# Performance work log

Measured on AMD Instinct MI355X. Metric: run time of the kernel, lower is better.

## Reference

```python
import jax, jax.numpy as jnp
import numpy as np

EPS = 1e-12  # matches torch F.normalize default eps


def _l2norm(x):
    n = jnp.linalg.norm(x, axis=-1, keepdims=True)
    return x / jnp.maximum(n, EPS)


def setup_inputs() -> dict:
    key = jax.random.key(0)
    k1, k2, k3, k4 = jax.random.split(key, 4)
    B, N, Lq, Ld, D = 64, 16, 32, 256, 128
    query_rep = jax.random.normal(k1, (B, Lq, D), jnp.float32)
    doc_reps = jax.random.normal(k2, (B, N, Ld, D), jnp.float32)
    doc_mask = jax.random.randint(k3, (B, N, Ld), 0, 2).astype(jnp.int32)
    labels = jax.random.normal(k4, (B, 2 * N), jnp.float32)
    return {"query_rep": query_rep, "doc_reps": doc_reps,
            "doc_mask": doc_mask, "labels": labels}


def reference(query_rep, doc_reps, doc_mask, labels):
    # ColBERT MaxSim: normalize query tokens (no mask, as in original),
    # mask+normalize doc tokens, bmm, max over doc tokens, sum over query tokens.
    q = _l2norm(query_rep)                                   # [B,Lq,D]
    d = _l2norm(doc_reps * doc_mask[..., None].astype(doc_reps.dtype))  # [B,N,Ld,D]
    tok = jnp.einsum('bqd,bnld->bnql', q, d)                 # [B,N,Lq,Ld]
    scores = tok.max(axis=-1).sum(axis=-1)                   # [B,N]

    # Pairwise ranking loss
    N = scores.shape[1]
    ys = labels[:, :N]
    idx = labels[:, N:]
    diffs = jnp.triu(scores[:, :, None] - scores[:, None, :])    # [B,N,N], lower tri zeroed
    weights = jnp.abs(idx[:, :, None] - idx[:, None, :])
    pairs = (ys[:, :, None] - ys[:, None, :]) > 0
    losses = jnp.log1p(jnp.exp(-diffs)) * weights
    return jnp.sum(jnp.where(pairs, losses, 0.0))
```

## Files before the change

### kernel.cpp

```cpp
#include <hip/hip_runtime.h>
#include <cmath>

#define EPSN 1e-12f

typedef _Float16 half8 __attribute__((ext_vector_type(8)));
typedef float f32x4 __attribute__((ext_vector_type(4)));

__global__ __launch_bounds__(256, 4) void scores_kernel(
    const float* __restrict__ qr, const float* __restrict__ doc,
    const int* __restrict__ mask, float* __restrict__ pmax) {
    __shared__ __align__(16) char Aimg[16384];
    __shared__ __align__(16) char Bimg[16384];
    __shared__ float ssPart[256];
    __shared__ float invS[128];
    __shared__ int   compactS[128];
    __shared__ int   cntW[2];
    __shared__ float wq[4][32];

    int t = threadIdx.x, g = blockIdx.x;
    int bn = g >> 1, h = g & 1, b = g >> 5;
    int w = t >> 6, lane = t & 63, col = lane & 15;

    int row = t >> 3, jb = t & 7;
    const float4* qsrc = (const float4*)(qr + ((size_t)b * 32 + row) * 128 + jb * 16);
    float4 v0 = qsrc[0], v1 = qsrc[1], v2 = qsrc[2], v3 = qsrc[3];

    int myMask = 0;
    if (t < 128) myMask = mask[bn * 256 + h * 128 + t];
    unsigned long long bal = __ballot(myMask != 0);
    if (t < 128 && lane == 0) cntW[w] = __popcll(bal);
    __syncthreads();
    int cnt = cntW[0] + cntW[1];
    if (myMask) {
        int prefix = __popcll(bal & ((1ull << lane) - 1));
        int basec = (w == 1) ? cntW[0] : 0;
        compactS[basec + prefix] = t;
    }
    __syncthreads();

    int s = t & 127, kh = t >> 7;
    bool real = (s < cnt);
    int tokc = real ? compactS[s] : 0;

    const float4* dsrc = (const float4*)(doc + ((size_t)bn * 256 + h * 128 + tokc) * 128) + kh * 4;
    float4 rA0, rA1, rA2, rA3, rB0, rB1, rB2, rB3, rC0, rC1, rC2, rC3;
    if (real) {
        rA0 = dsrc[0];  rA1 = dsrc[1];  rA2 = dsrc[2],  rA3 = dsrc[3];
        rB0 = dsrc[8];  rB1 = dsrc[9];  rB2 = dsrc[10]; rB3 = dsrc[11];
    }

    {
        float ss = v0.x*v0.x + v0.y*v0.y + v0.z*v0.z + v0.w*v0.w
                 + v1.x*v1.x + v1.y*v1.y + v1.z*v1.z + v1.w*v1.w
                 + v2.x*v2.x + v2.y*v2.y + v2.z*v2.z + v2.w*v2.w
                 + v3.x*v3.x + v3.y*v3.y + v3.z*v3.z + v3.w*v3.w;
        ss += __shfl_xor(ss, 1); ss += __shfl_xor(ss, 2); ss += __shfl_xor(ss, 4);
        float inv = 1.0f / fmaxf(sqrtf(ss), EPSN);
        int qt = row >> 4, kstep = jb >> 1;
        float4 vv[4] = { v0, v1, v2, v3 };
#pragma unroll
        for (int khh = 0; khh < 2; ++khh) {
            float xs[8] = { vv[2*khh].x,   vv[2*khh].y,   vv[2*khh].z,   vv[2*khh].w,
                            vv[2*khh+1].x, vv[2*khh+1].y, vv[2*khh+1].z, vv[2*khh+1].w };
            half8 hh, hl;
#pragma unroll
            for (int e = 0; e < 8; ++e) {
                float x = xs[e] * inv;
                _Float16 hv = (_Float16)x;
                hh[e] = hv;
                hl[e] = (_Float16)(x - (float)hv);
            }
            int quad = (jb & 1) * 2 + khh;
            int base = ((qt * 4 + kstep) * 2) * 1024 + ((row & 15) + quad * 16) * 16;
            *(half8*)(Aimg + base)        = hh;
            *(half8*)(Aimg + base + 1024) = hl;
        }
    }
    asm volatile("s_waitcnt lgkmcnt(0)" ::: "memory");
    __builtin_amdgcn_s_barrier();

    f32x4 acc[2][2];
    f32x4 zero = {0.f, 0.f, 0.f, 0.f};
    acc[0][0] = zero; acc[0][1] = zero; acc[1][0] = zero; acc[1][1] = zero;
    float ss_d = 0.f;

    int tile8 = s >> 4;
    int bo_base = tile8 * 2048 + (2 * kh) * 256 + (s & 15) * 16;

#define CHUNK(C, P0, P1, P2, P3, N0, N1, N2, N3, PREF, ISLAST) do {           \
    if ((PREF) && real) {                                                     \
        N0 = dsrc[(C + 2) * 8 + 0]; N1 = dsrc[(C + 2) * 8 + 1];               \
        N2 = dsrc[(C + 2) * 8 + 2]; N3 = dsrc[(C + 2) * 8 + 3];               \
    }                                                                         \
    if (real) {                                                               \
        ss_d += P0.x*P0.x + P0.y*P0.y + P0.z*P0.z + P0.w*P0.w;                \
        ss_d += P1.x*P1.x + P1.y*P1.y + P1.z*P1.z + P1.w*P1.w;                \
        ss_d += P2.x*P2.x + P2.y*P2.y + P2.z*P2.z + P2.w*P2.w;                \
        ss_d += P3.x*P3.x + P3.y*P3.y + P3.z*P3.z + P3.w*P3.w;                \
        float xa[8] = { P0.x, P0.y, P0.z, P0.w, P1.x, P1.y, P1.z, P1.w };     \
        float xb[8] = { P2.x, P2.y, P2.z, P2.w, P3.x, P3.y, P3.z, P3.w };     \
        half8 hha, hla, hhb, hlb;                                             \
        _Pragma("unroll")                                                     \
        for (int e = 0; e < 8; ++e) {                                         \
            float x = xa[e]; _Float16 hv = (_Float16)x;                       \
            hha[e] = hv; hla[e] = (_Float16)(x - (float)hv);                  \
            float y = xb[e]; _Float16 hw = (_Float16)y;                       \
            hhb[e] = hw; hlb[e] = (_Float16)(y - (float)hw);                  \
        }                                                                     \
        *(half8*)(Bimg + bo_base)              = hha;                         \
        *(half8*)(Bimg + bo_base + 1024)       = hla;                         \
        *(half8*)(Bimg + bo_base + 256)        = hhb;                         \
        *(half8*)(Bimg + bo_base + 256 + 1024) = hlb;                         \
    } else if ((C) == 0) {                                                    \
        half8 hz = {0,0,0,0,0,0,0,0};                                         \
        *(half8*)(Bimg + bo_base)              = hz;                          \
        *(half8*)(Bimg + bo_base + 1024)       = hz;                          \
        *(half8*)(Bimg + bo_base + 256)        = hz;                          \
        *(half8*)(Bimg + bo_base + 256 + 1024) = hz;                          \
    }                                                                         \
    if (ISLAST) ssPart[t] = ss_d;                                             \
    asm volatile("s_waitcnt lgkmcnt(0)" ::: "memory");                        \
    __builtin_amdgcn_s_barrier();                                             \
    if ((ISLAST) && t < 128) {                                                \
        float sst = ssPart[t] + ssPart[t + 128];                              \
        invS[t] = (t < cnt) ? (1.0f / fmaxf(sqrtf(sst), EPSN)) : 0.0f;        \
    }                                                                         \
    {                                                                         \
        int lo = lane << 4;                                                   \
        half8 a0h = *(const half8*)(Aimg + (((C) * 2 + 0) << 10) + lo);       \
        half8 a0l = *(const half8*)(Aimg + (((C) * 2 + 1) << 10) + lo);       \
        half8 a1h = *(const half8*)(Aimg + (((4 + (C)) * 2 + 0) << 10) + lo); \
        half8 a1l = *(const half8*)(Aimg + (((4 + (C)) * 2 + 1) << 10) + lo); \
        _Pragma("unroll")                                                     \
        for (int nt = 0; nt < 2; ++nt) {                                      \
            int tile = w * 2 + nt;                                            \
            half8 bh = *(const half8*)(Bimg + tile * 2048 + lo);              \
            half8 bl = *(const half8*)(Bimg + tile * 2048 + 1024 + lo);       \
            acc[0][nt] = __builtin_amdgcn_mfma_f32_16x16x32_f16(a0l, bh, acc[0][nt], 0, 0, 0); \
            acc[0][nt] = __builtin_amdgcn_mfma_f32_16x16x32_f16(a0h, bl, acc[0][nt], 0, 0, 0); \
            acc[0][nt] = __builtin_amdgcn_mfma_f32_16x16x32_f16(a0h, bh, acc[0][nt], 0, 0, 0); \
            acc[1][nt] = __builtin_amdgcn_mfma_f32_16x16x32_f16(a1l, bh, acc[1][nt], 0, 0, 0); \
            acc[1][nt] = __builtin_amdgcn_mfma_f32_16x16x32_f16(a1h, bl, acc[1][nt], 0, 0, 0); \
            acc[1][nt] = __builtin_amdgcn_mfma_f32_16x16x32_f16(a1h, bh, acc[1][nt], 0, 0, 0); \
        }                                                                     \
    }                                                                         \
    asm volatile("s_waitcnt lgkmcnt(0)" ::: "memory");                        \
    __builtin_amdgcn_s_barrier();                                             \
} while (0)

    CHUNK(0, rA0, rA1, rA2, rA3, rC0, rC1, rC2, rC3, 1, false);
    CHUNK(1, rB0, rB1, rB2, rB3, rA0, rA1, rA2, rA3, 1, false);
    CHUNK(2, rC0, rC1, rC2, rC3, rB0, rB1, rB2, rB3, 0, false);
    CHUNK(3, rA0, rA1, rA2, rA3, rB0, rB1, rB2, rB3, 0, true);
#undef CHUNK

    float inv0 = invS[w * 32 + col];
    float inv1 = invS[w * 32 + 16 + col];
    float m8[8];
#pragma unroll
    for (int qt = 0; qt < 2; ++qt)
#pragma unroll
        for (int rr = 0; rr < 4; ++rr)
            m8[qt * 4 + rr] = fmaxf(acc[qt][0][rr] * inv0, acc[qt][1][rr] * inv1);
#pragma unroll
    for (int off = 1; off < 16; off <<= 1)
#pragma unroll
        for (int i = 0; i < 8; ++i) m8[i] = fmaxf(m8[i], __shfl_xor(m8[i], off));
    if (col == 0) {
        int rg = lane >> 4;
#pragma unroll
        for (int qt = 0; qt < 2; ++qt)
#pragma unroll
            for (int rr = 0; rr < 4; ++rr) wq[w][qt * 16 + rg * 4 + rr] = m8[qt * 4 + rr];
    }
    __syncthreads();
    if (w == 0 && lane < 32) {
        float v = fmaxf(fmaxf(wq[0][lane], wq[1][lane]), fmaxf(wq[2][lane], wq[3][lane]));
        pmax[(size_t)g * 32 + lane] = v;
    }
}

__global__ __launch_bounds__(256) void lossb_kernel(const float* __restrict__ pmax,
                                                    const float* __restrict__ labels,
                                                    float* __restrict__ partial) {
    __shared__ float pmL[1024];
    __shared__ float sc[16], ysS[16], idxS[16];
    __shared__ float wsum[4];
    int b = blockIdx.x, t = threadIdx.x;
    ((float4*)pmL)[t] = ((const float4*)(pmax + (size_t)b * 1024))[t];
    if (t < 16) { ysS[t] = labels[b * 32 + t]; idxS[t] = labels[b * 32 + 16 + t]; }
    __syncthreads();
    {
        int n = t >> 4, qq = t & 15;
        float v = fmaxf(pmL[n * 64 + qq],      pmL[n * 64 + 32 + qq])
                + fmaxf(pmL[n * 64 + 16 + qq], pmL[n * 64 + 48 + qq]);
        v += __shfl_xor(v, 1); v += __shfl_xor(v, 2);
        v += __shfl_xor(v, 4); v += __shfl_xor(v, 8);
        if (qq == 0) sc[n] = v;
    }
    __syncthreads();
    int i = t >> 4, j = t & 15;
    float v = 0.f;
    if (ysS[i] - ysS[j] > 0.f) {
        float wgt = fabsf(idxS[i] - idxS[j]);
        float d = (i <= j) ? (sc[i] - sc[j]) : 0.f;
        v = log1pf(expf(-d)) * wgt;
    }
#pragma unroll
    for (int off = 1; off < 64; off <<= 1) v += __shfl_xor(v, off);
    int lane = t & 63;
    if (lane == 0) wsum[t >> 6] = v;
    __syncthreads();
    if (t == 0) partial[b] = wsum[0] + wsum[1] + wsum[2] + wsum[3];
}

__global__ void lossfin_kernel(const float* __restrict__ partial, float* __restrict__ out) {
    int t = threadIdx.x;
    float v = partial[t];
#pragma unroll
    for (int off = 1; off < 64; off <<= 1) v += __shfl_xor(v, off);
    if (t == 0) out[0] = v;
}

extern "C" void kernel_launch(void* const* d_in, const int* in_sizes, int n_in,
                              void* d_out, int out_size, void* d_ws, size_t ws_size,
                              hipStream_t stream) {
    const float* qr     = (const float*)d_in[0];
    const float* doc    = (const float*)d_in[1];
    const int*   dmask  = (const int*)d_in[2];
    const float* labels = (const float*)d_in[3];
    float* out = (float*)d_out;

    float* pmax    = (float*)d_ws;
    float* partial = pmax + 2048 * 32;

    scores_kernel<<<2048, 256, 0, stream>>>(qr, doc, dmask, pmax);
    lossb_kernel<<<64, 256, 0, stream>>>(pmax, labels, partial);
    lossfin_kernel<<<1, 64, 0, stream>>>(partial, out);
}
```

Before: 30.03 us.

## Process whole document per block and merge loss kernels into one

The scores kernel now runs one 512-thread block per (batch, document) that covers all 256 doc tokens, instead of two 256-thread blocks that each covered half. This lets it reduce the per-query max and the sum into one score inside the kernel, so no per-half max array is written. The two loss kernels are merged into a single 1024-thread block, removing one launch. The cost is larger blocks with twice the shared memory, which may lower occupancy, and a single-block loss stage that runs serially over all pairs.

```diff
diff --git a/kernel.cpp b/kernel.cpp
--- a/kernel.cpp
+++ b/kernel.cpp
@@ -6,50 +6,59 @@
 typedef _Float16 half8 __attribute__((ext_vector_type(8)));
 typedef float f32x4 __attribute__((ext_vector_type(4)));
 
-__global__ __launch_bounds__(256, 4) void scores_kernel(
+__global__ __launch_bounds__(512, 4) void scores_kernel(
     const float* __restrict__ qr, const float* __restrict__ doc,
-    const int* __restrict__ mask, float* __restrict__ pmax) {
+    const int* __restrict__ mask, float* __restrict__ scores) {
     __shared__ __align__(16) char Aimg[16384];
-    __shared__ __align__(16) char Bimg[16384];
-    __shared__ float ssPart[256];
-    __shared__ float invS[128];
-    __shared__ int   compactS[128];
-    __shared__ int   cntW[2];
-    __shared__ float wq[4][32];
+    __shared__ __align__(16) char Bimg[32768];
+    __shared__ float ssPart[512];
+    __shared__ float invS[256];
+    __shared__ int   compactS[256];
+    __shared__ int   cntW[4];
+    __shared__ float wq[8][32];
 
     int t = threadIdx.x, g = blockIdx.x;
-    int bn = g >> 1, h = g & 1, b = g >> 5;
+    int b = g >> 4;
     int w = t >> 6, lane = t & 63, col = lane & 15;
 
-    int row = t >> 3, jb = t & 7;
-    const float4* qsrc = (const float4*)(qr + ((size_t)b * 32 + row) * 128 + jb * 16);
-    float4 v0 = qsrc[0], v1 = qsrc[1], v2 = qsrc[2], v3 = qsrc[3];
+    int row = (t & 255) >> 3, jb = t & 7;
+    float4 v0, v1, v2, v3;
+    if (t < 256) {
+        const float4* qsrc = (const float4*)(qr + ((size_t)b * 32 + row) * 128 + jb * 16);
+        v0 = qsrc[0]; v1 = qsrc[1]; v2 = qsrc[2]; v3 = qsrc[3];
+    }
 
     int myMask = 0;
-    if (t < 128) myMask = mask[bn * 256 + h * 128 + t];
-    unsigned long long bal = __ballot(myMask != 0);
-    if (t < 128 && lane == 0) cntW[w] = __popcll(bal);
-    __syncthreads();
-    int cnt = cntW[0] + cntW[1];
+    unsigned long long bal = 0;
+    if (t < 256) {
+        myMask = mask[g * 256 + t];
+        bal = __ballot(myMask != 0);
+        if (lane == 0) cntW[w] = __popcll(bal);
+    }
+    __syncthreads();
+    int cnt = cntW[0] + cntW[1] + cntW[2] + cntW[3];
     if (myMask) {
         int prefix = __popcll(bal & ((1ull << lane) - 1));
-        int basec = (w == 1) ? cntW[0] : 0;
+        int basec = 0;
+        if (w >= 1) basec += cntW[0];
+        if (w >= 2) basec += cntW[1];
+        if (w >= 3) basec += cntW[2];
         compactS[basec + prefix] = t;
     }
     __syncthreads();
 
-    int s = t & 127, kh = t >> 7;
+    int s = t & 255, kh = t >> 8;
     bool real = (s < cnt);
     int tokc = real ? compactS[s] : 0;
 
-    const float4* dsrc = (const float4*)(doc + ((size_t)bn * 256 + h * 128 + tokc) * 128) + kh * 4;
+    const float4* dsrc = (const float4*)(doc + ((size_t)g * 256 + tokc) * 128) + kh * 4;
     float4 rA0, rA1, rA2, rA3, rB0, rB1, rB2, rB3, rC0, rC1, rC2, rC3;
     if (real) {
-        rA0 = dsrc[0];  rA1 = dsrc[1];  rA2 = dsrc[2],  rA3 = dsrc[3];
+        rA0 = dsrc[0];  rA1 = dsrc[1];  rA2 = dsrc[2];  rA3 = dsrc[3];
         rB0 = dsrc[8];  rB1 = dsrc[9];  rB2 = dsrc[10]; rB3 = dsrc[11];
     }
 
-    {
+    if (t < 256) {
         float ss = v0.x*v0.x + v0.y*v0.y + v0.z*v0.z + v0.w*v0.w
                  + v1.x*v1.x + v1.y*v1.y + v1.z*v1.z + v1.w*v1.w
                  + v2.x*v2.x + v2.y*v2.y + v2.z*v2.z + v2.w*v2.w
@@ -84,8 +93,7 @@
     acc[0][0] = zero; acc[0][1] = zero; acc[1][0] = zero; acc[1][1] = zero;
     float ss_d = 0.f;
 
-    int tile8 = s >> 4;
-    int bo_base = tile8 * 2048 + (2 * kh) * 256 + (s & 15) * 16;
+    int bo_base = (s >> 4) * 2048 + (2 * kh) * 256 + (s & 15) * 16;
 
 #define CHUNK(C, P0, P1, P2, P3, N0, N1, N2, N3, PREF, ISLAST) do {           \
     if ((PREF) && real) {                                                     \
@@ -121,8 +129,8 @@
     if (ISLAST) ssPart[t] = ss_d;                                             \
     asm volatile("s_waitcnt lgkmcnt(0)" ::: "memory");                        \
     __builtin_amdgcn_s_barrier();                                             \
-    if ((ISLAST) && t < 128) {                                                \
-        float sst = ssPart[t] + ssPart[t + 128];                              \
+    if ((ISLAST) && t < 256) {                                                \
+        float sst = ssPart[t] + ssPart[t + 256];                              \
         invS[t] = (t < cnt) ? (1.0f / fmaxf(sqrtf(sst), EPSN)) : 0.0f;        \
     }                                                                         \
     {                                                                         \
@@ -174,52 +182,53 @@
             for (int rr = 0; rr < 4; ++rr) wq[w][qt * 16 + rg * 4 + rr] = m8[qt * 4 + rr];
     }
     __syncthreads();
-    if (w == 0 && lane < 32) {
-        float v = fmaxf(fmaxf(wq[0][lane], wq[1][lane]), fmaxf(wq[2][lane], wq[3][lane]));
-        pmax[(size_t)g * 32 + lane] = v;
+    if (w == 0) {
+        float v = 0.f;
+        if (lane < 32) {
+            v = wq[0][lane];
+#pragma unroll
+            for (int ww = 1; ww < 8; ++ww) v = fmaxf(v, wq[ww][lane]);
+        }
+#pragma unroll
+        for (int off = 1; off < 64; off <<= 1) v += __shfl_xor(v, off);
+        if (lane == 0) scores[g] = v;
     }
 }
 
-__global__ __launch_bounds__(256) void lossb_kernel(const float* __restrict__ pmax,
+__global__ __launch_bounds__(1024) void loss_kernel(const float* __restrict__ scores,
                                                     const float* __restrict__ labels,
-                                                    float* __restrict__ partial) {
-    __shared__ float pmL[1024];
-    __shared__ float sc[16], ysS[16], idxS[16];
-    __shared__ float wsum[4];
-    int b = blockIdx.x, t = threadIdx.x;
-    ((float4*)pmL)[t] = ((const float4*)(pmax + (size_t)b * 1024))[t];
-    if (t < 16) { ysS[t] = labels[b * 32 + t]; idxS[t] = labels[b * 32 + 16 + t]; }
-    __syncthreads();
-    {
-        int n = t >> 4, qq = t & 15;
-        float v = fmaxf(pmL[n * 64 + qq],      pmL[n * 64 + 32 + qq])
-                + fmaxf(pmL[n * 64 + 16 + qq], pmL[n * 64 + 48 + qq]);
-        v += __shfl_xor(v, 1); v += __shfl_xor(v, 2);
-        v += __shfl_xor(v, 4); v += __shfl_xor(v, 8);
-        if (qq == 0) sc[n] = v;
-    }
-    __syncthreads();
-    int i = t >> 4, j = t & 15;
-    float v = 0.f;
-    if (ysS[i] - ysS[j] > 0.f) {
-        float wgt = fabsf(idxS[i] - idxS[j]);
-        float d = (i <= j) ? (sc[i] - sc[j]) : 0.f;
-        v = log1pf(expf(-d)) * wgt;
-    }
-#pragma unroll
-    for (int off = 1; off < 64; off <<= 1) v += __shfl_xor(v, off);
+                                                    float* __restrict__ out) {
+    __shared__ float scL[1024];
+    __shared__ float labL[2048];
+    __shared__ float wsum[16];
+    int t = threadIdx.x;
+    labL[t] = labels[t];
+    labL[t + 1024] = labels[t + 1024];
+    scL[t] = scores[t];
+    __syncthreads();
+    float total = 0.f;
+#pragma unroll
+    for (int it = 0; it < 16; ++it) {
+        int p = t + it * 1024;
+        int b = p >> 8, ij = p & 255, i = ij >> 4, j = ij & 15;
+        float ysi = labL[b * 32 + i], ysj = labL[b * 32 + j];
+        if (ysi - ysj > 0.f) {
+            float wgt = fabsf(labL[b * 32 + 16 + i] - labL[b * 32 + 16 + j]);
+            float d = (i <= j) ? (scL[b * 16 + i] - scL[b * 16 + j]) : 0.f;
+            total += log1pf(expf(-d)) * wgt;
+        }
+    }
+#pragma unroll
+    for (int off = 1; off < 64; off <<= 1) total += __shfl_xor(total, off);
     int lane = t & 63;
-    if (lane == 0) wsum[t >> 6] = v;
-    __syncthreads();
-    if (t == 0) partial[b] = wsum[0] + wsum[1] + wsum[2] + wsum[3];
-}
-
-__global__ void lossfin_kernel(const float* __restrict__ partial, float* __restrict__ out) {
-    int t = threadIdx.x;
-    float v = partial[t];
-#pragma unroll
-    for (int off = 1; off < 64; off <<= 1) v += __shfl_xor(v, off);
-    if (t == 0) out[0] = v;
+    if (lane == 0) wsum[t >> 6] = total;
+    __syncthreads();
+    if (t < 64) {
+        float v = (t < 16) ? wsum[t] : 0.f;
+#pragma unroll
+        for (int off = 1; off < 64; off <<= 1) v += __shfl_xor(v, off);
+        if (t == 0) out[0] = v;
+    }
 }
 
 extern "C" void kernel_launch(void* const* d_in, const int* in_sizes, int n_in,
@@ -231,10 +240,8 @@
     const float* labels = (const float*)d_in[3];
     float* out = (float*)d_out;
 
-    float* pmax    = (float*)d_ws;
-    float* partial = pmax + 2048 * 32;
-
-    scores_kernel<<<2048, 256, 0, stream>>>(qr, doc, dmask, pmax);
-    lossb_kernel<<<64, 256, 0, stream>>>(pmax, labels, partial);
-    lossfin_kernel<<<1, 64, 0, stream>>>(partial, out);
+    float* scores = (float*)d_ws;
+
+    scores_kernel<<<1024, 512, 0, stream>>>(qr, doc, dmask, scores);
+    loss_kernel<<<1, 1024, 0, stream>>>(scores, labels, out);
 }
```

After: 42.83 us. 1.43x slower.
